# Optimization experiments

Measured on AMD Instinct MI355X. Metric: run time of the kernel, lower is better.

The kernel has to match this reference:

```python
import jax, jax.numpy as jnp
import numpy as np

B, S, HID = 1, 2048, 2048
N_HEADS = 16
HEAD_DIM = HID // N_HEADS  # 128
ROPE_THETA = 10000.0
NEG_INF = -1e9


def setup_inputs() -> dict:
    key = jax.random.key(0)
    ks = jax.random.split(key, 5)
    hidden_states = jax.random.normal(ks[0], (B, S, HID), dtype=jnp.float32)
    scale = 1.0 / np.sqrt(HID)
    Wq = jax.random.normal(ks[1], (HID, HID), dtype=jnp.float32) * scale
    Wk = jax.random.normal(ks[2], (HID, HID), dtype=jnp.float32) * scale
    Wv = jax.random.normal(ks[3], (HID, HID), dtype=jnp.float32) * scale
    Wo = jax.random.normal(ks[4], (HID, HID), dtype=jnp.float32) * scale
    # additive causal mask [B, 1, S, S]: 0 on/below diag, -1e9 above
    causal = jnp.tril(jnp.ones((S, S), dtype=bool))
    attention_mask = jnp.where(causal, 0.0, NEG_INF).astype(jnp.float32)[None, None]
    attention_mask = jnp.broadcast_to(attention_mask, (B, 1, S, S))
    position_ids = jnp.broadcast_to(jnp.arange(S, dtype=jnp.int64)[None, :], (B, S))
    return {"hidden_states": hidden_states, "Wq": Wq, "Wk": Wk, "Wv": Wv,
            "Wo": Wo, "attention_mask": attention_mask, "position_ids": position_ids}


def _rotate_half(x):
    x1, x2 = jnp.split(x, 2, axis=-1)
    return jnp.concatenate((-x2, x1), axis=-1)


def _rope_cos_sin(position_ids, head_dim, dtype):
    inv_freq = 1.0 / (ROPE_THETA ** (jnp.arange(0, head_dim, 2, dtype=jnp.float32) / head_dim))
    freqs = position_ids.astype(jnp.float32)[:, :, None] * inv_freq[None, None, :]  # [b, s, d/2]
    emb = jnp.concatenate((freqs, freqs), axis=-1)  # [b, s, d]
    # unsqueeze_dim=1 -> broadcast over heads
    return jnp.cos(emb).astype(dtype)[:, None], jnp.sin(emb).astype(dtype)[:, None]


def reference(hidden_states, Wq, Wk, Wv, Wo, attention_mask, position_ids):
    b, s, h = hidden_states.shape
    d = HEAD_DIM
    def proj(W):
        return (hidden_states @ W.T).reshape(b, s, N_HEADS, d).transpose(0, 2, 1, 3)  # [b,h,s,d]
    q, k, v = proj(Wq), proj(Wk), proj(Wv)
    cos, sin = _rope_cos_sin(position_ids, d, q.dtype)
    q = q * cos + _rotate_half(q) * sin
    k = k * cos + _rotate_half(k) * sin
    scores = jnp.einsum('bhqd,bhkd->bhqk', q, k) / jnp.sqrt(jnp.float32(d))
    scores = scores + attention_mask
    probs = jax.nn.softmax(scores.astype(jnp.float32), axis=-1).astype(q.dtype)
    attn = jnp.einsum('bhqk,bhkd->bhqd', probs, v)
    out = attn.transpose(0, 2, 1, 3).reshape(b, s, h)
    return out @ Wo.T
```

## Files before the change

kernel.cpp:

```cpp
#include <hip/hip_runtime.h>

typedef _Float16 half8 __attribute__((ext_vector_type(8)));
typedef _Float16 half4 __attribute__((ext_vector_type(4)));
typedef float floatx4 __attribute__((ext_vector_type(4)));
typedef float floatx16 __attribute__((ext_vector_type(16)));

#define GLDS(gp, lp) __builtin_amdgcn_global_load_lds( \
    (const __attribute__((address_space(1))) void*)(gp), \
    (__attribute__((address_space(3))) void*)(lp), 16, 0, 0)

__global__ void cvt_f2h5(const float* __restrict__ s0, const float* __restrict__ s1,
                         const float* __restrict__ s2, const float* __restrict__ s3,
                         const float* __restrict__ s4,
                         _Float16* __restrict__ d0, _Float16* __restrict__ d1,
                         _Float16* __restrict__ d2, _Float16* __restrict__ d3,
                         _Float16* __restrict__ d4, int n8) {
  int i = blockIdx.x * 256 + threadIdx.x;
  if (i >= n8) return;
  const float* s; _Float16* d;
  switch (blockIdx.y) {
    case 0: s = s0; d = d0; break;
    case 1: s = s1; d = d1; break;
    case 2: s = s2; d = d2; break;
    case 3: s = s3; d = d3; break;
    default: s = s4; d = d4; break;
  }
  const float4* s4p = (const float4*)s;
  float4 a = s4p[2 * i], b = s4p[2 * i + 1];
  half8 h;
  h[0] = (_Float16)a.x; h[1] = (_Float16)a.y; h[2] = (_Float16)a.z; h[3] = (_Float16)a.w;
  h[4] = (_Float16)b.x; h[5] = (_Float16)b.y; h[6] = (_Float16)b.z; h[7] = (_Float16)b.w;
  *(half8*)(d + 8 * (size_t)i) = h;
}

__global__ __launch_bounds__(256) void rope_tr(_Float16* __restrict__ K,
                                               const _Float16* __restrict__ V,
                                               _Float16* __restrict__ Vt) {
  __shared__ _Float16 t[64][72];
  const int bid = (int)blockIdx.x;
  if (bid < 8192) {
    const int idx = bid * 256 + threadIdx.x;
    const int s = idx >> 10;
    const int hd = idx & 1023;
    const int head = hd >> 6, d = hd & 63;
    const float freq = exp2f((float)d * -0.2076205059304601f);
    const float ang = (float)s * freq;
    float sn, c;
    __sincosf(ang, &sn, &c);
    const size_t base = (size_t)s * 2048 + head * 128 + d;
    float k1 = (float)K[base], k2 = (float)K[base + 64];
    K[base]      = (_Float16)(k1 * c - k2 * sn);
    K[base + 64] = (_Float16)(k2 * c + k1 * sn);
  } else {
    const int b2 = bid - 8192;
    const int r0 = (b2 >> 5) * 64, c0 = (b2 & 31) * 64;
    const int tr = threadIdx.x >> 3, tc = (threadIdx.x & 7) * 8;
    #pragma unroll
    for (int p = 0; p < 2; ++p) {
      half8 v = *(const half8*)(V + (size_t)(r0 + p * 32 + tr) * 2048 + c0 + tc);
      *(half8*)&t[p * 32 + tr][tc] = v;
    }
    __syncthreads();
    #pragma unroll
    for (int p = 0; p < 2; ++p) {
      half8 v;
      #pragma unroll
      for (int j = 0; j < 8; ++j) v[j] = t[tc + j][p * 32 + tr];
      *(half8*)(Vt + (size_t)(c0 + p * 32 + tr) * 2048 + r0 + tc) = v;
    }
  }
}

__global__ __launch_bounds__(512, 1) void gemm_qkv(const _Float16* __restrict__ A,
                                                   const _Float16* __restrict__ W,
                                                   _Float16* __restrict__ Cq) {
  extern __shared__ _Float16 lds[];
  _Float16* As = lds;
  _Float16* Bs = lds + 3 * 16384;

  const int tid = threadIdx.x, lane = tid & 63, wv = tid >> 6;
  const int fr = lane & 15, fg = lane >> 4;
  const int wm = wv >> 1, wn = wv & 1;
  const int bm = blockIdx.y * 256, bn = blockIdx.x * 192;
  const _Float16* Ab = A + (size_t)bm * 2048;
  const _Float16* Bb = W + (size_t)bn * 2048;

  const int srow = lane >> 3;
  const int sgr = (lane & 7) ^ srow;

  auto stageA = [&](int t) {
    _Float16* dst = As + (t % 3) * 16384;
    const size_t coff = (size_t)t * 64 + sgr * 8;
    #pragma unroll
    for (int i = 0; i < 4; ++i) {
      const int rb = wv * 32 + i * 8;
      GLDS(Ab + (size_t)(rb + srow) * 2048 + coff, dst + rb * 64);
    }
  };
  auto stageB = [&](int t) {
    _Float16* dst = Bs + (t & 1) * 12288;
    const size_t coff = (size_t)t * 64 + sgr * 8;
    #pragma unroll
    for (int i = 0; i < 3; ++i) {
      const int rb = wv * 24 + i * 8;
      GLDS(Bb + (size_t)(rb + srow) * 2048 + coff, dst + rb * 64);
    }
  };

  const int arow = wm * 64 + fr;
  const int brow = wn * 96 + fr;
  const int sw = fr & 7;

  floatx4 acc[4][6] = {};

  stageA(0); stageB(0); stageA(1);
  asm volatile("s_waitcnt vmcnt(4)" ::: "memory");
  __builtin_amdgcn_s_barrier();

  for (int t = 0; t < 32; ++t) {
    const _Float16* Ac = As + (t % 3) * 16384;
    const _Float16* Bc = Bs + (t & 1) * 12288;
    half8 af[2][4], bf[2][6];
    #pragma unroll
    for (int kh = 0; kh < 2; ++kh) {
      const int sl = ((kh * 4 + fg) ^ sw) * 8;
      #pragma unroll
      for (int m = 0; m < 4; ++m)
        af[kh][m] = *(const half8*)(Ac + (arow + m * 16) * 64 + sl);
      #pragma unroll
      for (int n = 0; n < 6; ++n)
        bf[kh][n] = *(const half8*)(Bc + (brow + n * 16) * 64 + sl);
    }
    if (t + 1 < 32) stageB(t + 1);
    if (t + 2 < 32) stageA(t + 2);
    __builtin_amdgcn_s_setprio(1);
    #pragma unroll
    for (int kh = 0; kh < 2; ++kh)
      #pragma unroll
      for (int m = 0; m < 4; ++m)
        #pragma unroll
        for (int n = 0; n < 6; ++n)
          acc[m][n] = __builtin_amdgcn_mfma_f32_16x16x32_f16(af[kh][m], bf[kh][n],
                                                             acc[m][n], 0, 0, 0);
    __builtin_amdgcn_s_setprio(0);
    if (t < 30)       asm volatile("s_waitcnt vmcnt(4)" ::: "memory");
    else if (t == 30) asm volatile("s_waitcnt vmcnt(0)" ::: "memory");
    __builtin_amdgcn_s_barrier();
  }

  #pragma unroll
  for (int m = 0; m < 4; ++m)
    #pragma unroll
    for (int n = 0; n < 6; ++n)
      #pragma unroll
      for (int i = 0; i < 4; ++i) {
        const int row = bm + wm * 64 + m * 16 + fg * 4 + i;
        const int col = bn + wn * 96 + n * 16 + fr;
        Cq[(size_t)(col >> 11) * 4194304 + (size_t)row * 2048 + (col & 2047)] =
            (_Float16)acc[m][n][i];
      }
}

__global__ __launch_bounds__(256, 3) void gemm_o(const _Float16* __restrict__ A,
                                                 const _Float16* __restrict__ B,
                                                 float* __restrict__ out) {
  extern __shared__ _Float16 lds[];
  _Float16* As = lds;
  _Float16* Bs = lds + 3 * 4096;

  const int tid = threadIdx.x, lane = tid & 63, wv = tid >> 6;
  const int fr = lane & 15, fg = lane >> 4;
  const int wm = (wv >> 1) * 64, wn = (wv & 1) * 64;
  const int bm = blockIdx.y * 128, bn = blockIdx.x * 128;
  const _Float16* Ab = A + (size_t)bm * 2048;
  const _Float16* Bb = B + (size_t)bn * 2048;

  const int srow = lane >> 2;
  const int gsw = (lane & 3) ^ ((lane >> 3) & 3);
  const int asw = (fr >> 1) & 3;

  auto stageA = [&](int t) {
    _Float16* dst = As + (t % 3) * 4096;
    const size_t coff = (size_t)t * 32 + gsw * 8;
    #pragma unroll
    for (int i = 0; i < 2; ++i) {
      const int rb = wv * 32 + i * 16;
      GLDS(Ab + (size_t)(rb + srow) * 2048 + coff, dst + rb * 32);
    }
  };
  auto stageB = [&](int t) {
    _Float16* dst = Bs + (t % 3) * 4096;
    const size_t coff = (size_t)t * 32 + gsw * 8;
    #pragma unroll
    for (int i = 0; i < 2; ++i) {
      const int rb = wv * 32 + i * 16;
      GLDS(Bb + (size_t)(rb + srow) * 2048 + coff, dst + rb * 32);
    }
  };

  floatx4 acc[4][4] = {};

  stageA(0); stageB(0); stageA(1); stageB(1);
  asm volatile("s_waitcnt vmcnt(4)" ::: "memory");
  __builtin_amdgcn_s_barrier();

  for (int t = 0; t < 64; ++t) {
    const _Float16* Ac = As + (t % 3) * 4096;
    const _Float16* Bc = Bs + (t % 3) * 4096;
    half8 af[4], bf[4];
    #pragma unroll
    for (int m = 0; m < 4; ++m)
      af[m] = *(const half8*)(Ac + (wm + m * 16 + fr) * 32 + ((fg ^ asw) * 8));
    #pragma unroll
    for (int n = 0; n < 4; ++n)
      bf[n] = *(const half8*)(Bc + (wn + n * 16 + fr) * 32 + ((fg ^ asw) * 8));
    if (t + 2 < 64) { stageA(t + 2); stageB(t + 2); }
    __builtin_amdgcn_s_setprio(1);
    #pragma unroll
    for (int m = 0; m < 4; ++m)
      #pragma unroll
      for (int n = 0; n < 4; ++n)
        acc[m][n] = __builtin_amdgcn_mfma_f32_16x16x32_f16(af[m], bf[n], acc[m][n], 0, 0, 0);
    __builtin_amdgcn_s_setprio(0);
    if (t < 62) asm volatile("s_waitcnt vmcnt(4)" ::: "memory");
    else        asm volatile("s_waitcnt vmcnt(0)" ::: "memory");
    __builtin_amdgcn_s_barrier();
  }

  #pragma unroll
  for (int m = 0; m < 4; ++m)
    #pragma unroll
    for (int n = 0; n < 4; ++n)
      #pragma unroll
      for (int i = 0; i < 4; ++i) {
        const int row = bm + wm + m * 16 + fg * 4 + i;
        const int col = bn + wn + n * 16 + fr;
        out[(size_t)row * 2048 + col] = acc[m][n][i];
      }
}

__global__ __launch_bounds__(256, 2) void attn_k(const _Float16* __restrict__ Qp,
                                                 const _Float16* __restrict__ Kp,
                                                 const _Float16* __restrict__ Vt,
                                                 _Float16* __restrict__ Po,
                                                 float* __restrict__ Pr,
                                                 _Float16* __restrict__ At) {
  extern __shared__ _Float16 smem[];
  _Float16* Ks = smem;
  _Float16* Vs = smem + 2 * 64 * 128;
  _Float16* Pb = smem + 4 * 64 * 128;

  const int tid = threadIdx.x, lane = tid & 63, wv = tid >> 6;
  const int l31 = lane & 31, hi = lane >> 5;
  const int wq = wv >> 1, wk = wv & 1;

  const int bid = (int)blockIdx.x;
  const int head = ((bid & 7) << 1) | ((bid >> 3) & 1);
  const int L = bid >> 4;
  int g, it0, itEnd;
  if (L < 16) { g = 16 + L; it0 = 0; itEnd = 16; }
  else {
    const int j = (L - 16) >> 1;
    if ((L & 1) == 0) { g = 15 - j; it0 = 0; itEnd = g + 1; }
    else             { g = 31 - j; it0 = 16; itEnd = g + 1; }
  }
  const bool full = (it0 == 0) && (itEnd == g + 1);
  const size_t hoff = (size_t)head * 128;
  const int qw = g * 64 + wq * 32;
  _Float16* Pw = Pb + wv * (32 * 40);

  half8 qf[8];
  #pragma unroll
  for (int ks = 0; ks < 8; ++ks)
    qf[ks] = *(const half8*)(Qp + (size_t)(qw + l31) * 2048 + hoff + ks * 16 + hi * 8);
  {
    const float qrow = (float)(qw + l31);
    #pragma unroll
    for (int ks = 0; ks < 4; ++ks)
      #pragma unroll
      for (int j = 0; j < 8; ++j) {
        const int d = ks * 16 + hi * 8 + j;
        const float fq = exp2f((float)d * -0.2076205059304601f);
        float sn, c;
        __sincosf(qrow * fq, &sn, &c);
        const float q0 = (float)qf[ks][j], q1 = (float)qf[ks + 4][j];
        qf[ks][j]     = (_Float16)((q0 * c - q1 * sn) * 0.08838834764831845f);
        qf[ks + 4][j] = (_Float16)((q1 * c + q0 * sn) * 0.08838834764831845f);
      }
  }

  auto stage = [&](int buf, int it) {
    const int kv0 = it * 64;
    #pragma unroll
    for (int i = 0; i < 4; ++i) {
      const int rbase = wv * 16 + i * 4;
      const int row = rbase + (lane >> 4);
      const int gr = (lane & 15) ^ (row & 7);
      GLDS(Kp + (size_t)(kv0 + row) * 2048 + hoff + gr * 8,
           Ks + buf * 8192 + rbase * 128);
    }
    #pragma unroll
    for (int i = 0; i < 4; ++i) {
      const int rbase = wv * 32 + i * 8;
      const int row = rbase + (lane >> 3);
      const int gr = (lane & 7) ^ (row & 7);
      GLDS(Vt + (size_t)(hoff + row) * 2048 + kv0 + gr * 8,
           Vs + buf * 8192 + rbase * 64);
    }
  };

  floatx16 o[4] = {};
  float rsum = 0.0f;

  stage(0, it0);
  asm volatile("s_waitcnt vmcnt(0)" ::: "memory");
  __builtin_amdgcn_s_barrier();

  int buf = 0;
  for (int it = it0; it < itEnd; ++it) {
    if (it + 1 < itEnd) stage(buf ^ 1, it + 1);
    const _Float16* Kb = Ks + buf * 8192;
    const _Float16* Vb = Vs + buf * 8192;

    const int krow = wk * 32 + l31;
    const int ksw = l31 & 7;
    floatx16 S = {};
    __builtin_amdgcn_s_setprio(1);
    #pragma unroll
    for (int ks = 0; ks < 8; ++ks) {
      half8 a = *(const half8*)(Kb + krow * 128 + (((ks * 2 + hi) ^ ksw) * 8));
      S = __builtin_amdgcn_mfma_f32_32x32x16_f16(a, qf[ks], S, 0, 0, 0);
    }
    __builtin_amdgcn_s_setprio(0);

    if (it == g) {
      const int kv0 = it * 64;
      const int qa = qw + l31;
      #pragma unroll
      for (int r = 0; r < 16; ++r) {
        const int ka = kv0 + wk * 32 + (r & 3) + 8 * (r >> 2) + 4 * hi;
        if (ka > qa) S[r] = -1e30f;
      }
    }

    #pragma unroll
    for (int r4 = 0; r4 < 4; ++r4) {
      float p0 = __expf(S[4 * r4 + 0] - 8.0f);
      float p1 = __expf(S[4 * r4 + 1] - 8.0f);
      float p2 = __expf(S[4 * r4 + 2] - 8.0f);
      float p3 = __expf(S[4 * r4 + 3] - 8.0f);
      rsum += (p0 + p1) + (p2 + p3);
      half4 pk;
      pk[0] = (_Float16)p0; pk[1] = (_Float16)p1;
      pk[2] = (_Float16)p2; pk[3] = (_Float16)p3;
      *(half4*)(Pw + l31 * 40 + r4 * 8 + hi * 4) = pk;
    }

    half8 pa0 = *(const half8*)(Pw + l31 * 40 + hi * 8);
    half8 pa1 = *(const half8*)(Pw + l31 * 40 + 16 + hi * 8);

    __builtin_amdgcn_s_setprio(1);
    #pragma unroll
    for (int dt = 0; dt < 4; ++dt) {
      const int vrow = dt * 32 + l31;
      const int vsw = vrow & 7;
      half8 b0 = *(const half8*)(Vb + vrow * 64 + (((wk * 4 + hi) ^ vsw) * 8));
      half8 b1 = *(const half8*)(Vb + vrow * 64 + (((wk * 4 + 2 + hi) ^ vsw) * 8));
      o[dt] = __builtin_amdgcn_mfma_f32_32x32x16_f16(pa0, b0, o[dt], 0, 0, 0);
      o[dt] = __builtin_amdgcn_mfma_f32_32x32x16_f16(pa1, b1, o[dt], 0, 0, 0);
    }
    __builtin_amdgcn_s_setprio(0);

    asm volatile("s_waitcnt vmcnt(0)" ::: "memory");
    __builtin_amdgcn_s_barrier();
    buf ^= 1;
  }

  float* Mo = (float*)smem;
  float* Mr = (float*)(smem + 16384);
  if (wk == 1) {
    #pragma unroll
    for (int dt = 0; dt < 4; ++dt)
      #pragma unroll
      for (int r = 0; r < 16; ++r)
        Mo[((wq * 4 + dt) * 16 + r) * 64 + lane] = o[dt][r];
    Mr[wq * 64 + lane] = rsum;
  }
  __syncthreads();
  if (wk == 0) {
    rsum += Mr[wq * 64 + lane];
    float rs = rsum;
    rs += __shfl_xor(rs, 32);
    if (full) {
      const float inv = 1.0f / rs;
      float invq[16];
      #pragma unroll
      for (int r = 0; r < 16; ++r)
        invq[r] = __shfl(inv, (r & 3) + 8 * (r >> 2) + 4 * hi, 32);
      #pragma unroll
      for (int dt = 0; dt < 4; ++dt)
        #pragma unroll
        for (int r = 0; r < 16; ++r) {
          const float w = (o[dt][r] + Mo[((wq * 4 + dt) * 16 + r) * 64 + lane]) * invq[r];
          const int qa = qw + (r & 3) + 8 * (r >> 2) + 4 * hi;
          At[(size_t)qa * 2048 + hoff + dt * 32 + l31] = (_Float16)w;
        }
    } else {
      if (hi == 0) Pr[(size_t)bid * 64 + wq * 32 + l31] = rs;
      #pragma unroll
      for (int dt = 0; dt < 4; ++dt)
        #pragma unroll
        for (int r = 0; r < 16; ++r) {
          const float w = o[dt][r] + Mo[((wq * 4 + dt) * 16 + r) * 64 + lane];
          const int ql = wq * 32 + (r & 3) + 8 * (r >> 2) + 4 * hi;
          Po[(size_t)bid * 8192 + ql * 128 + dt * 32 + l31] = (_Float16)w;
        }
    }
  }
}

__global__ __launch_bounds__(256) void attn_merge(const _Float16* __restrict__ Po,
                                                  const float* __restrict__ Pr,
                                                  _Float16* __restrict__ At) {
  const int bidx = (int)blockIdx.x;
  const int h = bidx & 15, g = 16 + (bidx >> 4);
  const int hb = ((h & 1) << 3) | (h >> 1);
  const int U0 = (g - 16) * 16 + hb;
  const int U1 = (17 + 2 * (31 - g)) * 16 + hb;
  const int t = threadIdx.x;
  const int q = t >> 2, cs = t & 3;
  const float r0 = Pr[(size_t)U0 * 64 + q];
  const float r1 = Pr[(size_t)U1 * 64 + q];
  const float inv = 1.0f / (r0 + r1);
  const size_t orow = (size_t)(g * 64 + q) * 2048 + h * 128;
  #pragma unroll
  for (int s = 0; s < 4; ++s) {
    const int d0 = (cs + s * 4) * 8;
    half8 a = *(const half8*)(Po + (size_t)U0 * 8192 + q * 128 + d0);
    half8 b = *(const half8*)(Po + (size_t)U1 * 8192 + q * 128 + d0);
    half8 o;
    #pragma unroll
    for (int j = 0; j < 8; ++j) o[j] = (_Float16)(((float)a[j] + (float)b[j]) * inv);
    *(half8*)(At + orow + d0) = o;
  }
}

extern "C" void kernel_launch(void* const* d_in, const int* in_sizes, int n_in,
                              void* d_out, int out_size, void* d_ws, size_t ws_size,
                              hipStream_t stream) {
  (void)in_sizes; (void)n_in; (void)out_size; (void)ws_size;
  const float* X  = (const float*)d_in[0];
  const float* Wq = (const float*)d_in[1];
  const float* Wk = (const float*)d_in[2];
  const float* Wv = (const float*)d_in[3];
  const float* Wo = (const float*)d_in[4];
  float* out = (float*)d_out;

  const size_t SZ = 2048ull * 2048ull;
  _Float16* ws  = (_Float16*)d_ws;
  _Float16* Xh  = ws + 0 * SZ;
  _Float16* Wqh = ws + 1 * SZ;
  _Float16* Wkh = ws + 2 * SZ;
  _Float16* Wvh = ws + 3 * SZ;
  _Float16* Woh = ws + 4 * SZ;
  _Float16* Qp  = ws + 5 * SZ;
  _Float16* Kp  = ws + 6 * SZ;
  _Float16* Vp  = ws + 7 * SZ;
  _Float16* Vtg = Wqh;
  _Float16* At  = Xh;
  _Float16* Po  = Wkh;
  float*    Pr  = (float*)Vp;

  const int n8 = (int)(SZ / 8);
  dim3 blk(256);

  cvt_f2h5<<<dim3(n8 / 256, 5), blk, 0, stream>>>(X, Wq, Wk, Wv, Wo,
                                                  Xh, Wqh, Wkh, Wvh, Woh, n8);

  gemm_qkv<<<dim3(32, 8), dim3(512), 147456, stream>>>(Xh, Wqh, Qp);

  rope_tr<<<8192 + 1024, blk, 0, stream>>>(Kp, Vp, Vtg);

  const size_t attn_lds = (4 * 64 * 128 + 4 * 32 * 40) * sizeof(_Float16);
  attn_k<<<768, blk, attn_lds, stream>>>(Qp, Kp, Vtg, Po, Pr, At);
  attn_merge<<<256, blk, 0, stream>>>(Po, Pr, At);

  gemm_o<<<dim3(16, 16), blk, 49152, stream>>>(At, Woh, out);
}
```

Baseline: 150.3 us.

## Switch QKV GEMM to 32x32x16 MFMA with 4 waves and larger per-wave tiles

The QKV projection GEMM now runs 256 threads (4 waves) per block instead of 512. Each wave computes a 128x96 tile using 32x32x16 MFMA instructions in place of 16x16x32, with a new XOR swizzle for the LDS layout and a reworked epilogue. The aim is fewer LDS fragment reads per MFMA and better instruction efficiency. In exchange, each wave holds more accumulator registers, fewer waves are available to hide latency, and each thread issues twice as many global-to-LDS loads.

```diff
diff --git a/kernel.cpp b/kernel.cpp
--- a/kernel.cpp
+++ b/kernel.cpp
@@ -71,7 +71,7 @@
   }
 }
 
-__global__ __launch_bounds__(512, 1) void gemm_qkv(const _Float16* __restrict__ A,
+__global__ __launch_bounds__(256, 1) void gemm_qkv(const _Float16* __restrict__ A,
                                                    const _Float16* __restrict__ W,
                                                    _Float16* __restrict__ Cq) {
   extern __shared__ _Float16 lds[];
@@ -79,86 +79,96 @@
   _Float16* Bs = lds + 3 * 16384;
 
   const int tid = threadIdx.x, lane = tid & 63, wv = tid >> 6;
-  const int fr = lane & 15, fg = lane >> 4;
+  const int l31 = lane & 31, hi = lane >> 5;
   const int wm = wv >> 1, wn = wv & 1;
   const int bm = blockIdx.y * 256, bn = blockIdx.x * 192;
   const _Float16* Ab = A + (size_t)bm * 2048;
   const _Float16* Bb = W + (size_t)bn * 2048;
 
   const int srow = lane >> 3;
-  const int sgr = (lane & 7) ^ srow;
 
   auto stageA = [&](int t) {
     _Float16* dst = As + (t % 3) * 16384;
-    const size_t coff = (size_t)t * 64 + sgr * 8;
-    #pragma unroll
-    for (int i = 0; i < 4; ++i) {
-      const int rb = wv * 32 + i * 8;
-      GLDS(Ab + (size_t)(rb + srow) * 2048 + coff, dst + rb * 64);
+    #pragma unroll
+    for (int i = 0; i < 8; ++i) {
+      const int rb = wv * 64 + i * 8;
+      const int gr = (lane & 7) ^ srow ^ (((rb + srow) >> 2) & 6);
+      GLDS(Ab + (size_t)(rb + srow) * 2048 + t * 64 + gr * 8, dst + rb * 64);
     }
   };
   auto stageB = [&](int t) {
     _Float16* dst = Bs + (t & 1) * 12288;
-    const size_t coff = (size_t)t * 64 + sgr * 8;
-    #pragma unroll
-    for (int i = 0; i < 3; ++i) {
-      const int rb = wv * 24 + i * 8;
-      GLDS(Bb + (size_t)(rb + srow) * 2048 + coff, dst + rb * 64);
+    #pragma unroll
+    for (int i = 0; i < 6; ++i) {
+      const int rb = wv * 48 + i * 8;
+      const int gr = (lane & 7) ^ srow ^ (((rb + srow) >> 2) & 6);
+      GLDS(Bb + (size_t)(rb + srow) * 2048 + t * 64 + gr * 8, dst + rb * 64);
     }
   };
 
-  const int arow = wm * 64 + fr;
-  const int brow = wn * 96 + fr;
-  const int sw = fr & 7;
-
-  floatx4 acc[4][6] = {};
+  const int rsw = (l31 & 7) ^ ((l31 >> 2) & 6);
+
+  floatx16 acc[2][3] = {};
+  floatx16 acc2[2][3] = {};
 
   stageA(0); stageB(0); stageA(1);
-  asm volatile("s_waitcnt vmcnt(4)" ::: "memory");
+  asm volatile("s_waitcnt vmcnt(8)" ::: "memory");
   __builtin_amdgcn_s_barrier();
+
+  const int arow = wm * 128 + l31;
+  const int brow = wn * 96 + l31;
 
   for (int t = 0; t < 32; ++t) {
     const _Float16* Ac = As + (t % 3) * 16384;
     const _Float16* Bc = Bs + (t & 1) * 12288;
-    half8 af[2][4], bf[2][6];
-    #pragma unroll
-    for (int kh = 0; kh < 2; ++kh) {
-      const int sl = ((kh * 4 + fg) ^ sw) * 8;
-      #pragma unroll
-      for (int m = 0; m < 4; ++m)
-        af[kh][m] = *(const half8*)(Ac + (arow + m * 16) * 64 + sl);
-      #pragma unroll
-      for (int n = 0; n < 6; ++n)
-        bf[kh][n] = *(const half8*)(Bc + (brow + n * 16) * 64 + sl);
+    half8 af[4][4], bf[4][3];
+    #pragma unroll
+    for (int ks = 0; ks < 4; ++ks) {
+      const int sl = (((ks * 2 + hi) ^ rsw) & 7) * 8;
+      #pragma unroll
+      for (int mb = 0; mb < 4; ++mb)
+        af[ks][mb] = *(const half8*)(Ac + (arow + mb * 32) * 64 + sl);
+      #pragma unroll
+      for (int nb = 0; nb < 3; ++nb)
+        bf[ks][nb] = *(const half8*)(Bc + (brow + nb * 32) * 64 + sl);
     }
     if (t + 1 < 32) stageB(t + 1);
     if (t + 2 < 32) stageA(t + 2);
     __builtin_amdgcn_s_setprio(1);
     #pragma unroll
-    for (int kh = 0; kh < 2; ++kh)
-      #pragma unroll
-      for (int m = 0; m < 4; ++m)
+    for (int ks = 0; ks < 4; ++ks) {
+      #pragma unroll
+      for (int mb = 0; mb < 2; ++mb)
         #pragma unroll
-        for (int n = 0; n < 6; ++n)
-          acc[m][n] = __builtin_amdgcn_mfma_f32_16x16x32_f16(af[kh][m], bf[kh][n],
-                                                             acc[m][n], 0, 0, 0);
+        for (int nb = 0; nb < 3; ++nb)
+          acc[mb][nb] = __builtin_amdgcn_mfma_f32_32x32x16_f16(af[ks][mb], bf[ks][nb],
+                                                               acc[mb][nb], 0, 0, 0);
+      #pragma unroll
+      for (int mb = 0; mb < 2; ++mb)
+        #pragma unroll
+        for (int nb = 0; nb < 3; ++nb)
+          acc2[mb][nb] = __builtin_amdgcn_mfma_f32_32x32x16_f16(af[ks][mb + 2], bf[ks][nb],
+                                                                acc2[mb][nb], 0, 0, 0);
+    }
     __builtin_amdgcn_s_setprio(0);
-    if (t < 30)       asm volatile("s_waitcnt vmcnt(4)" ::: "memory");
+    if (t < 30)       asm volatile("s_waitcnt vmcnt(8)" ::: "memory");
     else if (t == 30) asm volatile("s_waitcnt vmcnt(0)" ::: "memory");
     __builtin_amdgcn_s_barrier();
   }
 
   #pragma unroll
-  for (int m = 0; m < 4; ++m)
-    #pragma unroll
-    for (int n = 0; n < 6; ++n)
-      #pragma unroll
-      for (int i = 0; i < 4; ++i) {
-        const int row = bm + wm * 64 + m * 16 + fg * 4 + i;
-        const int col = bn + wn * 96 + n * 16 + fr;
+  for (int mb = 0; mb < 4; ++mb)
+    #pragma unroll
+    for (int nb = 0; nb < 3; ++nb) {
+      const floatx16& a = (mb < 2) ? acc[mb][nb] : acc2[mb - 2][nb];
+      #pragma unroll
+      for (int r = 0; r < 16; ++r) {
+        const int row = bm + wm * 128 + mb * 32 + (r & 3) + 8 * (r >> 2) + 4 * hi;
+        const int col = bn + wn * 96 + nb * 32 + l31;
         Cq[(size_t)(col >> 11) * 4194304 + (size_t)row * 2048 + (col & 2047)] =
-            (_Float16)acc[m][n][i];
+            (_Float16)a[r];
       }
+    }
 }
 
 __global__ __launch_bounds__(256, 3) void gemm_o(const _Float16* __restrict__ A,
@@ -477,7 +487,7 @@
   cvt_f2h5<<<dim3(n8 / 256, 5), blk, 0, stream>>>(X, Wq, Wk, Wv, Wo,
                                                   Xh, Wqh, Wkh, Wvh, Woh, n8);
 
-  gemm_qkv<<<dim3(32, 8), dim3(512), 147456, stream>>>(Xh, Wqh, Qp);
+  gemm_qkv<<<dim3(32, 8), blk, 147456, stream>>>(Xh, Wqh, Qp);
 
   rope_tr<<<8192 + 1024, blk, 0, stream>>>(Kp, Vp, Vtg);
 
```

Measured after the change: 155.0 us. 3.1% more time.
